# Kernel optimization log

Hardware: AMD Instinct MI355X
Metric: run time of the kernel (lower is better)

## Reference

```python
import jax, jax.numpy as jnp
import numpy as np

K = 3            # kernel size
C_IN = 8
C_OUT = 16
PATCH = C_IN * K * K  # 72
EPS = 1e-6


def setup_inputs() -> dict:
    key = jax.random.key(0)
    k1, k2, k3 = jax.random.split(key, 3)
    in_tensor = jax.random.normal(k1, (4, C_IN, 112, 112), dtype=jnp.float32)
    # 1x1-conv weighting predictor: C_in -> PATCH*C_OUT channels
    w_pred = jax.random.normal(k2, (PATCH * C_OUT, C_IN), dtype=jnp.float32) * 0.05
    b_pred = jax.random.normal(k3, (PATCH * C_OUT,), dtype=jnp.float32) * 0.05
    return {"in_tensor": in_tensor, "w_pred": w_pred, "b_pred": b_pred}


def reference(in_tensor, w_pred, b_pred):
    B, C, H, W = in_tensor.shape
    # --- weighting module: predict dynamic weights per spatial location ---
    raw = jnp.einsum('bchw,oc->bohw', in_tensor, w_pred) + b_pred[None, :, None, None]
    weightings = raw.reshape(B, PATCH, C_OUT, H, W)          # [B, C*k*k, C_out, H, W]
    # norm = L2 norm of the dynamic weight over the patch dim -> [B, C_out, H, W]
    norm = jnp.sqrt(jnp.sum(weightings * weightings, axis=1)) + EPS
    # --- unfold: overlapping k x k patches, same padding, stride 1 ---
    patches = jax.lax.conv_general_dilated_patches(
        in_tensor, (K, K), (1, 1), 'SAME')                   # [B, C*k*k, H, W]
    # --- weighted sum over the patch dim, then normalize ---
    activations = jnp.einsum('bphw,bpohw->bohw', patches, weightings)  # [B, C_out, H, W]
    return activations / norm
```

## Files before the change

kernel.cpp:

```cpp
#include <hip/hip_runtime.h>
#include <math.h>

#define IMG_W 112
#define HW    12544
#define CI    8
#define CO    16
#define NP    72
#define EPS   1e-6f

typedef __attribute__((ext_vector_type(8))) short short8;
typedef __attribute__((ext_vector_type(4))) float f32x4;

static __device__ inline short f2bf(float f) {
  unsigned u = __float_as_uint(f);
  return (short)((u + 0x7FFFu + ((u >> 16) & 1u)) >> 16);
}

__global__ __launch_bounds__(256) void coda_mfma(
    const float* __restrict__ in, const float* __restrict__ wp,
    const float* __restrict__ bp, float* __restrict__ out)
{
  __shared__ short sA[NP][32][8];
  __shared__ float sIn[CI][290];
  __shared__ short sZ[16];

  const int tid = threadIdx.x;
  const int b   = blockIdx.x / 196;
  const int r0  = (blockIdx.x - b * 196) * 64;
  const float* __restrict__ inb = in + b * CI * HW;

  for (int idx = tid; idx < NP * 32; idx += 256) {
    const int p = idx >> 5, l = idx & 31, q = l >> 4, m = l & 15;
    const int row = p * 16 + m;
    short8 v = {0, 0, 0, 0, 0, 0, 0, 0};
    if (q == 0) {
      const float* wr = wp + row * CI;
#pragma unroll
      for (int j = 0; j < 8; ++j) v[j] = f2bf(wr[j]);
    } else {
      v[0] = f2bf(bp[row]);
    }
    *(short8*)&sA[p][l][0] = v;
  }
  if (tid < 16) sZ[tid] = 0;
  for (int k = tid; k < CI * 290; k += 256) {
    const int c = k / 290;
    const int i = k - c * 290;
    int g = r0 - 113 + i;
    g = (g < 0) ? 0 : (g > HW - 1 ? HW - 1 : g);
    sIn[c][i] = inb[c * HW + g];
  }
  __syncthreads();

  const int wib  = tid >> 6;
  const int lane = tid & 63;
  const int ln   = lane & 15;
  const int quad = lane >> 4;
  const int rwav = r0 + wib * 16;
  const int h    = rwav / IMG_W;
  const int wl   = (rwav - h * IMG_W) + ln;
  const int off  = wib * 16 + ln + 113;

  float vm[9];
#pragma unroll
  for (int q = 0; q < 9; ++q) {
    const int kh = q / 3, kw = q % 3;
    const bool ok = ((unsigned)(h + kh - 1) < 112u) &&
                    ((unsigned)(wl + kw - 1) < 112u);
    vm[q] = ok ? 1.f : 0.f;
  }

  short8 bf = {0, 0, 0, 0, 0, 0, 0, 0};
#pragma unroll
  for (int j = 0; j < 8; ++j) {
    const short bv = f2bf(sIn[j][off]);
    bf[j] = (quad == 0) ? bv : ((quad == 1 && j == 0) ? (short)0x3F80 : (short)0);
  }

  float acc[4] = {0.f, 0.f, 0.f, 0.f};
  float n2[4]  = {0.f, 0.f, 0.f, 0.f};
  const bool qlo = (quad < 2);

#pragma unroll 1
  for (int c = 0; c < CI; ++c) {
    const float* __restrict__ sc = &sIn[c][off];
#pragma unroll
    for (int q = 0; q < 9; ++q) {
      static const int dq[9] = {-113, -112, -111, -1, 0, 1, 111, 112, 113};
      const int p = c * 9 + q;
      const short* ap = qlo ? &sA[p][quad * 16 + ln][0] : &sZ[0];
      const short8 af = *(const short8*)ap;
      const float pv = vm[q] * sc[dq[q]];
      const f32x4 zc = {0.f, 0.f, 0.f, 0.f};
      const f32x4 d = __builtin_amdgcn_mfma_f32_16x16x32_bf16(af, bf, zc, 0, 0, 0);
#pragma unroll
      for (int i = 0; i < 4; ++i) {
        acc[i] = fmaf(pv, d[i], acc[i]);
        n2[i]  = fmaf(d[i], d[i], n2[i]);
      }
    }
  }

  float* __restrict__ ob = out + (long)b * CO * HW + rwav + ln;
#pragma unroll
  for (int i = 0; i < 4; ++i) {
    const int co = quad * 4 + i;
    ob[(long)co * HW] = acc[i] / (sqrtf(n2[i]) + EPS);
  }
}

extern "C" void kernel_launch(void* const* d_in, const int* in_sizes, int n_in,
                              void* d_out, int out_size, void* d_ws, size_t ws_size,
                              hipStream_t stream) {
  const float* in = (const float*)d_in[0];
  const float* wp = (const float*)d_in[1];
  const float* bp = (const float*)d_in[2];
  float* out = (float*)d_out;

  coda_mfma<<<dim3(784), dim3(256), 0, stream>>>(in, wp, bp, out);
}
```

Measured before the change: 78.52 us.

## Split input-channel loop across two wave groups and reduce partials via LDS

The block grows to 512 threads so that two sets of four waves each process half of the 8 input channels for the same 64 output pixels. Their partial accumulators and squared-norm sums are then combined through shared memory before the normalized write. The channel loop is now fully unrolled. This doubles wave-level parallelism per block to hide MFMA and LDS latency, at the cost of two extra barriers, an LDS reduction, and idle waves during the final store.

Result: faster. 72.11 us (-8.2%).

```diff
diff --git a/kernel.cpp b/kernel.cpp
--- a/kernel.cpp
+++ b/kernel.cpp
@@ -16,12 +16,14 @@
   return (short)((u + 0x7FFFu + ((u >> 16) & 1u)) >> 16);
 }
 
-__global__ __launch_bounds__(256) void coda_mfma(
+static constexpr int DQ[9] = {-113, -112, -111, -1, 0, 1, 111, 112, 113};
+
+__global__ __launch_bounds__(512) void coda_mfma(
     const float* __restrict__ in, const float* __restrict__ wp,
     const float* __restrict__ bp, float* __restrict__ out)
 {
   __shared__ short sA[NP][32][8];
-  __shared__ float sIn[CI][290];
+  __shared__ float sBuf[CI * 290];
   __shared__ short sZ[16];
 
   const int tid = threadIdx.x;
@@ -29,7 +31,7 @@
   const int r0  = (blockIdx.x - b * 196) * 64;
   const float* __restrict__ inb = in + b * CI * HW;
 
-  for (int idx = tid; idx < NP * 32; idx += 256) {
+  for (int idx = tid; idx < NP * 32; idx += 512) {
     const int p = idx >> 5, l = idx & 31, q = l >> 4, m = l & 15;
     const int row = p * 16 + m;
     short8 v = {0, 0, 0, 0, 0, 0, 0, 0};
@@ -43,23 +45,25 @@
     *(short8*)&sA[p][l][0] = v;
   }
   if (tid < 16) sZ[tid] = 0;
-  for (int k = tid; k < CI * 290; k += 256) {
+  for (int k = tid; k < CI * 290; k += 512) {
     const int c = k / 290;
     const int i = k - c * 290;
-    int g = r0 - 113 + i;
-    g = (g < 0) ? 0 : (g > HW - 1 ? HW - 1 : g);
-    sIn[c][i] = inb[c * HW + g];
+    int gg = r0 - 113 + i;
+    gg = (gg < 0) ? 0 : (gg > HW - 1 ? HW - 1 : gg);
+    sBuf[k] = inb[c * HW + gg];
   }
   __syncthreads();
 
-  const int wib  = tid >> 6;
+  const int wave = tid >> 6;
   const int lane = tid & 63;
+  const int g    = wave & 3;
+  const int half = wave >> 2;
   const int ln   = lane & 15;
   const int quad = lane >> 4;
-  const int rwav = r0 + wib * 16;
+  const int rwav = r0 + g * 16;
   const int h    = rwav / IMG_W;
   const int wl   = (rwav - h * IMG_W) + ln;
-  const int off  = wib * 16 + ln + 113;
+  const int off  = g * 16 + ln + 113;
 
   float vm[9];
 #pragma unroll
@@ -73,24 +77,25 @@
   short8 bf = {0, 0, 0, 0, 0, 0, 0, 0};
 #pragma unroll
   for (int j = 0; j < 8; ++j) {
-    const short bv = f2bf(sIn[j][off]);
+    const short bv = f2bf(sBuf[j * 290 + off]);
     bf[j] = (quad == 0) ? bv : ((quad == 1 && j == 0) ? (short)0x3F80 : (short)0);
   }
 
   float acc[4] = {0.f, 0.f, 0.f, 0.f};
   float n2[4]  = {0.f, 0.f, 0.f, 0.f};
   const bool qlo = (quad < 2);
+  const int  c0  = half * 4;
 
-#pragma unroll 1
-  for (int c = 0; c < CI; ++c) {
-    const float* __restrict__ sc = &sIn[c][off];
+#pragma unroll
+  for (int cc = 0; cc < 4; ++cc) {
+    const int c = c0 + cc;
+    const float* __restrict__ sc = &sBuf[c * 290 + off];
 #pragma unroll
     for (int q = 0; q < 9; ++q) {
-      static const int dq[9] = {-113, -112, -111, -1, 0, 1, 111, 112, 113};
       const int p = c * 9 + q;
       const short* ap = qlo ? &sA[p][quad * 16 + ln][0] : &sZ[0];
       const short8 af = *(const short8*)ap;
-      const float pv = vm[q] * sc[dq[q]];
+      const float pv = vm[q] * sc[DQ[q]];
       const f32x4 zc = {0.f, 0.f, 0.f, 0.f};
       const f32x4 d = __builtin_amdgcn_mfma_f32_16x16x32_bf16(af, bf, zc, 0, 0, 0);
 #pragma unroll
@@ -101,11 +106,24 @@
     }
   }
 
-  float* __restrict__ ob = out + (long)b * CO * HW + rwav + ln;
+  __syncthreads();
+  if (half == 1) {
 #pragma unroll
-  for (int i = 0; i < 4; ++i) {
-    const int co = quad * 4 + i;
-    ob[(long)co * HW] = acc[i] / (sqrtf(n2[i]) + EPS);
+    for (int i = 0; i < 4; ++i) {
+      sBuf[i * 256 + g * 64 + lane]       = acc[i];
+      sBuf[(i + 4) * 256 + g * 64 + lane] = n2[i];
+    }
+  }
+  __syncthreads();
+  if (half == 0) {
+    float* __restrict__ ob = out + (long)b * CO * HW + rwav + ln;
+#pragma unroll
+    for (int i = 0; i < 4; ++i) {
+      const float a2 = acc[i] + sBuf[i * 256 + g * 64 + lane];
+      const float s2 = n2[i] + sBuf[(i + 4) * 256 + g * 64 + lane];
+      const int co = quad * 4 + i;
+      ob[(long)co * HW] = a2 / (sqrtf(s2) + EPS);
+    }
   }
 }
 
@@ -117,5 +135,5 @@
   const float* bp = (const float*)d_in[2];
   float* out = (float*)d_out;
 
-  coda_mfma<<<dim3(784), dim3(256), 0, stream>>>(in, wp, bp, out);
+  coda_mfma<<<dim3(784), dim3(512), 0, stream>>>(in, wp, bp, out);
 }
```
